# Performance work log

Measured on AMD Instinct MI355X. Metric: run time of the kernel, lower is better.

The kernel has to match this reference:

```python
import jax, jax.numpy as jnp
import numpy as np

B, NP, FIN = 128, 64, 2048   # graphs, nodes per graph, input feat
H, D = 8, 64                 # GAT heads, per-head dim
HD = H * D                   # 512
HID = 1024                   # Set2Set channels (concat of two 512 convs)
R2 = 16.0                    # radius^2 (r=4)
SLOPE = 0.2                  # GATConv leaky_relu slope
EPS = 0.1                    # BatchNorm eps


def setup_inputs() -> dict:
    key = jax.random.key(0)
    ks = jax.random.split(key, 20)
    s = 0.02
    inp = {}
    inp['x'] = jax.random.normal(ks[0], (B * NP, FIN), jnp.float32)
    inp['pos'] = jax.random.uniform(ks[1], (B * NP, 2), jnp.float32) * 20.0
    inp['batch'] = jnp.repeat(jnp.arange(B, dtype=jnp.int32), NP)
    # lin01: Linear(2048,2048,bias=False) + BN(2048, eps=0.1) (eval mode)
    inp['W0'] = jax.random.normal(ks[2], (FIN, 2048), jnp.float32) * s
    inp['bn0_g'] = jnp.ones((2048,), jnp.float32)
    inp['bn0_b'] = jnp.zeros((2048,), jnp.float32)
    inp['bn0_m'] = jnp.zeros((2048,), jnp.float32)
    inp['bn0_v'] = jnp.ones((2048,), jnp.float32)
    # two GATConv(2048, 64, heads=8)
    inp['Wg1'] = jax.random.normal(ks[3], (2048, HD), jnp.float32) * s
    inp['as1'] = jax.random.normal(ks[4], (H, D), jnp.float32) * s
    inp['ad1'] = jax.random.normal(ks[5], (H, D), jnp.float32) * s
    inp['b1'] = jnp.zeros((HD,), jnp.float32)
    inp['Wg2'] = jax.random.normal(ks[6], (2048, HD), jnp.float32) * s
    inp['as2'] = jax.random.normal(ks[7], (H, D), jnp.float32) * s
    inp['ad2'] = jax.random.normal(ks[8], (H, D), jnp.float32) * s
    inp['b2'] = jnp.zeros((HD,), jnp.float32)
    # Set2Set LSTM: 2 layers, input 2*HID, hidden HID
    inp['Wih0'] = jax.random.normal(ks[9], (4 * HID, 2 * HID), jnp.float32) * s
    inp['Whh0'] = jax.random.normal(ks[10], (4 * HID, HID), jnp.float32) * s
    inp['bih0'] = jnp.zeros((4 * HID,), jnp.float32)
    inp['bhh0'] = jnp.zeros((4 * HID,), jnp.float32)
    inp['Wih1'] = jax.random.normal(ks[11], (4 * HID, HID), jnp.float32) * s
    inp['Whh1'] = jax.random.normal(ks[12], (4 * HID, HID), jnp.float32) * s
    inp['bih1'] = jnp.zeros((4 * HID,), jnp.float32)
    inp['bhh1'] = jnp.zeros((4 * HID,), jnp.float32)
    # lin2: Linear(2048,1024,bias=False) + BN(1024, eps=0.1)
    inp['W2'] = jax.random.normal(ks[13], (2 * HID, HID), jnp.float32) * s
    inp['bn2_g'] = jnp.ones((HID,), jnp.float32)
    inp['bn2_b'] = jnp.zeros((HID,), jnp.float32)
    inp['bn2_m'] = jnp.zeros((HID,), jnp.float32)
    inp['bn2_v'] = jnp.ones((HID,), jnp.float32)
    # lin3: Linear(1024, 10)
    inp['W3'] = jax.random.normal(ks[14], (HID, 10), jnp.float32) * s
    inp['b3'] = jnp.zeros((10,), jnp.float32)
    return inp


def _bn(x, g, b, m, v):
    return (x - m) * jax.lax.rsqrt(v + EPS) * g + b


def _gat(xb, adj, Wg, a_src, a_dst, bias):
    # xb: [B, NP, 2048], adj: [B, NP, NP] bool (diag True = self-loops)
    h = (xb @ Wg).reshape(B, NP, H, D)
    es = jnp.einsum('bnhd,hd->bnh', h, a_src)   # source-node score
    ed = jnp.einsum('bnhd,hd->bnh', h, a_dst)   # target-node score
    # e[b, i, j, h]: edge j -> i
    e = jax.nn.leaky_relu(ed[:, :, None, :] + es[:, None, :, :], SLOPE)
    e = jnp.where(adj[..., None], e, -jnp.inf)
    alpha = jax.nn.softmax(e, axis=2)           # softmax over neighbors j
    out = jnp.einsum('bijh,bjhd->bihd', alpha, h).reshape(B, NP, HD)
    return out + bias


def _cell(inp, h, c, Wih, Whh, bih, bhh):
    z = inp @ Wih.T + h @ Whh.T + bih + bhh
    i, f, g, o = jnp.split(z, 4, axis=-1)
    c = jax.nn.sigmoid(f) * c + jax.nn.sigmoid(i) * jnp.tanh(g)
    return jax.nn.sigmoid(o) * jnp.tanh(c), c


def _forward(x, pos, W0, bn0_g, bn0_b, bn0_m, bn0_v,
             Wg1, as1, ad1, b1, Wg2, as2, ad2, b2,
             Wih0, Whh0, bih0, bhh0, Wih1, Whh1, bih1, bhh1,
             W2, bn2_g, bn2_b, bn2_m, bn2_v, W3, b3):
    # radius_graph(r=4) per graph; GATConv re-adds self-loops -> diag True
    p = pos.reshape(B, NP, 2)
    d2 = jnp.sum((p[:, :, None, :] - p[:, None, :, :]) ** 2, axis=-1)
    adj = d2 <= R2
    x = _bn(jax.nn.relu(x @ W0), bn0_g, bn0_b, bn0_m, bn0_v)  # dropout: eval
    xb = x.reshape(B, NP, 2048)
    g1 = jax.nn.relu(_gat(xb, adj, Wg1, as1, ad1, b1))
    g2 = jax.nn.relu(_gat(xb, adj, Wg2, as2, ad2, b2))
    x2 = jnp.concatenate([g1, g2], axis=-1)                   # [B, NP, 1024]
    # Set2Set: processing_steps=2, 2-layer LSTM
    q_star = jnp.zeros((B, 2 * HID), x2.dtype)
    h0 = c0 = h1 = c1 = jnp.zeros((B, HID), x2.dtype)
    for _ in range(2):
        h0, c0 = _cell(q_star, h0, c0, Wih0, Whh0, bih0, bhh0)
        h1, c1 = _cell(h0, h1, c1, Wih1, Whh1, bih1, bhh1)
        e = jnp.einsum('bnd,bd->bn', x2, h1)
        a = jax.nn.softmax(e, axis=1)                         # per-graph softmax
        r = jnp.einsum('bn,bnd->bd', a, x2)
        q_star = jnp.concatenate([h1, r], axis=-1)            # [B, 2048]
    y = _bn(jax.nn.relu(q_star @ W2), bn2_g, bn2_b, bn2_m, bn2_v)
    return y @ W3 + b3                                        # [B, 10] ('A2')


def reference(x, pos, batch, W0, bn0_g, bn0_b, bn0_m, bn0_v,
              Wg1, as1, ad1, b1, Wg2, as2, ad2, b2,
              Wih0, Whh0, bih0, bhh0, Wih1, Whh1, bih1, bhh1,
              W2, bn2_g, bn2_b, bn2_m, bn2_v, W3, b3):
    # batch ids are implicit in the fixed [B, NP] layout
    return _forward(x, pos, W0, bn0_g, bn0_b, bn0_m, bn0_v,
                    Wg1, as1, ad1, b1, Wg2, as2, ad2, b2,
                    Wih0, Whh0, bih0, bhh0, Wih1, Whh1, bih1, bhh1,
                    W2, bn2_g, bn2_b, bn2_m, bn2_v, W3, b3)
```

## Files before the change

kernel.cpp:

```cpp
#include <hip/hip_runtime.h>
#include <hip/hip_bf16.h>

typedef unsigned short u16;
typedef __attribute__((ext_vector_type(8))) short short8;
typedef __attribute__((ext_vector_type(4))) float f32x4;
typedef unsigned long long u64;

#define DI __device__ __forceinline__

DI u16 f2b(float f){
  unsigned u = __float_as_uint(f);
  unsigned r = 0x7fffu + ((u >> 16) & 1u);
  return (u16)((u + r) >> 16);
}
DI float b2f(u16 u){ return __uint_as_float((unsigned)u << 16); }

DI void gl_lds16(const void* g, void* l){
  __builtin_amdgcn_global_load_lds((const __attribute__((address_space(1))) void*)g,
                                   (__attribute__((address_space(3))) void*)l, 16, 0, 0);
}

constexpr size_t O_XBF = 0;
constexpr size_t O_W0T = O_XBF + 33554432;
constexpr size_t O_WGT = O_W0T + 8388608;
constexpr size_t O_W2T = O_WGT + 4194304;
constexpr size_t O_XB  = O_W2T + 4194304;
constexpr size_t O_H   = O_XB  + 33554432;
constexpr size_t O_ES  = O_H   + 33554432;
constexpr size_t O_ED  = O_ES  + 524288;
constexpr size_t O_ADJ = O_ED  + 524288;
constexpr size_t O_SC0 = O_ADJ + 65536;
constexpr size_t O_SH0 = O_SC0 + 8192;
constexpr size_t O_SC2 = O_SH0 + 8192;
constexpr size_t O_SH2 = O_SC2 + 4096;
constexpr size_t O_LB0 = O_SH2 + 4096;
constexpr size_t O_LB1 = O_LB0 + 16384;
constexpr size_t S_AC0 = 0;
constexpr size_t S_AC1 = S_AC0 + 786432;
constexpr size_t S_C0  = S_AC1 + 524288;
constexpr size_t S_C1  = S_C0  + 524288;
constexpr size_t S_H1F = S_C1  + 524288;
constexpr size_t S_ZP  = S_H1F + 524288;
constexpr size_t S_E   = S_ZP  + 16777216;
constexpr size_t S_Z1U = S_E   + 32768;

__global__ __launch_bounds__(256) void setup_all(
    const float* __restrict__ x,
    const float* __restrict__ W0, const float* __restrict__ Wg1,
    const float* __restrict__ Wg2, const float* __restrict__ W2,
    const float* __restrict__ g0, const float* __restrict__ b0, const float* __restrict__ m0, const float* __restrict__ v0,
    const float* __restrict__ g2, const float* __restrict__ b2, const float* __restrict__ m2, const float* __restrict__ v2,
    const float* __restrict__ bih0, const float* __restrict__ bhh0,
    const float* __restrict__ bih1, const float* __restrict__ bhh1,
    const float* __restrict__ pos,
    u16* __restrict__ xbf, u16* __restrict__ w0t, u16* __restrict__ wgt, u16* __restrict__ w2t,
    float* __restrict__ sc0, float* __restrict__ sh0, float* __restrict__ sc2, float* __restrict__ sh2,
    float* __restrict__ lb0, float* __restrict__ lb1, u64* __restrict__ adjm)
{
  __shared__ float tile[32][33];
  __shared__ float px[4][64], py[4][64];
  int bx = blockIdx.x, t = threadIdx.x;
  if(bx < 8192){
    int idx = bx * 256 + t;
    int r = idx >> 8, c8 = (idx & 255) << 3;
    const float* src = x + (size_t)r * 2048 + c8;
    float4 v0 = *(const float4*)src;
    float4 v1 = *(const float4*)(src + 4);
    short8 ov;
    ov[0] = (short)f2b(v0.x); ov[1] = (short)f2b(v0.y); ov[2] = (short)f2b(v0.z); ov[3] = (short)f2b(v0.w);
    ov[4] = (short)f2b(v1.x); ov[5] = (short)f2b(v1.y); ov[6] = (short)f2b(v1.z); ov[7] = (short)f2b(v1.w);
    *(short8*)(xbf + (size_t)r * 2048 + c8) = ov;
  } else if(bx < 16384){
    int bx2 = bx - 8192;
    int cx = bx2 & 127, by = bx2 >> 7;
    const float* src; u16* dst; int C, droff;
    if(cx < 64){      src = W0;  dst = w0t; C = 2048; droff = 0; }
    else if(cx < 80){ src = Wg1; dst = wgt; C = 512;  droff = 0;   cx -= 64; }
    else if(cx < 96){ src = Wg2; dst = wgt; C = 512;  droff = 512; cx -= 80; }
    else {            src = W2;  dst = w2t; C = 1024; droff = 0;   cx -= 96; }
    int c0 = cx * 32, r0 = by * 32;
    int tx = t & 31, ty = t >> 5;
    for(int i = 0; i < 4; i++)
      tile[ty + 8*i][tx] = src[(size_t)(r0 + ty + 8*i) * C + c0 + tx];
    __syncthreads();
    for(int i = 0; i < 4; i++)
      dst[(size_t)(droff + c0 + ty + 8*i) * 2048 + r0 + tx] = f2b(tile[tx][ty + 8*i]);
  } else if(bx < 16400){
    int tt = (bx - 16384) * 256 + t;
    if(tt < 2048){ float s = g0[tt] * rsqrtf(v0[tt] + 0.1f); sc0[tt] = s; sh0[tt] = b0[tt] - m0[tt] * s; }
    if(tt < 1024){ float s = g2[tt] * rsqrtf(v2[tt] + 0.1f); sc2[tt] = s; sh2[tt] = b2[tt] - m2[tt] * s; }
    lb0[tt] = bih0[tt] + bhh0[tt];
    lb1[tt] = bih1[tt] + bhh1[tt];
  } else {
    int w = t >> 6, l = t & 63;
    int g = (bx - 16400) * 4 + w;
    float2 p = ((const float2*)pos)[g * 64 + l];
    px[w][l] = p.x; py[w][l] = p.y;
    __syncthreads();
    float xi = p.x, yi = p.y;
    u64 m = 0;
    for(int j = 0; j < 64; j++){
      float dx = xi - px[w][j], dy = yi - py[w][j];
      if(dx * dx + dy * dy <= 16.0f) m |= (1ull << j);
    }
    adjm[g * 64 + l] = m;
  }
}

#define STAGE_A(buf, half, kt)                                                        \
  { _Pragma("unroll")                                                                 \
    for(int ld = 0; ld < 2; ld++){                                                    \
      int u = ld * 512 + t;                                                           \
      int r = (u >> 3) + (half) * 128, c = u & 7;                                     \
      gl_lds16(A + (size_t)(m0 + r) * K + (kt) * 64 + ((c ^ (r & 7)) << 3),           \
               LA + (buf) * 16384 + ((half) * 1024 + u) * 8);                         \
    } }
#define STAGE_B(buf, half, kt)                                                        \
  { _Pragma("unroll")                                                                 \
    for(int ld = 0; ld < 2; ld++){                                                    \
      int u = ld * 512 + t;                                                           \
      int r = (u >> 3) + (half) * 128, c = u & 7;                                     \
      gl_lds16(Bt + (size_t)(n0 + r) * K + (kt) * 64 + ((c ^ (r & 7)) << 3),          \
               LB + (buf) * 16384 + ((half) * 1024 + u) * 8);                         \
    } }
#define COMPUTE(buf, q)                                                               \
  { if((q) == 0){                                                                     \
      _Pragma("unroll")                                                               \
      for(int nb = 0; nb < 4; nb++)                                                   \
        _Pragma("unroll")                                                             \
        for(int k2 = 0; k2 < 2; k2++){                                                \
          int col = wn + nb * 16 + (l & 15);                                          \
          int kc = k2 * 4 + (l >> 4);                                                 \
          bfr[nb][k2] = Bp[(buf) * 2048 + col * 8 + (kc ^ (col & 7))];                \
        }                                                                             \
    }                                                                                 \
    short8 af[2][2];                                                                  \
    _Pragma("unroll")                                                                 \
    for(int rb = 0; rb < 2; rb++)                                                     \
      _Pragma("unroll")                                                               \
      for(int k2 = 0; k2 < 2; k2++){                                                  \
        int row = wm + (q) * 32 + rb * 16 + (l & 15);                                 \
        int kc = k2 * 4 + (l >> 4);                                                   \
        af[rb][k2] = Ap[(buf) * 2048 + row * 8 + (kc ^ (row & 7))];                   \
      }                                                                               \
    _Pragma("unroll")                                                                 \
    for(int rb = 0; rb < 2; rb++)                                                     \
      _Pragma("unroll")                                                               \
      for(int nb = 0; nb < 4; nb++)                                                   \
        _Pragma("unroll")                                                             \
        for(int k2 = 0; k2 < 2; k2++)                                                 \
          acc[(q) * 2 + rb][nb] = __builtin_amdgcn_mfma_f32_16x16x32_bf16(            \
              af[rb][k2], bfr[nb][k2], acc[(q) * 2 + rb][nb], 0, 0, 0);               \
  }
#define PHASE_BAR() { __builtin_amdgcn_s_barrier(); __builtin_amdgcn_sched_barrier(0); }
#define VM4() { asm volatile("s_waitcnt vmcnt(4)" ::: "memory"); __builtin_amdgcn_sched_barrier(0); }

__global__ __launch_bounds__(512, 2) void gemm8p(
    const u16* __restrict__ A, const u16* __restrict__ Bt, u16* __restrict__ Cb,
    const float* __restrict__ p1, const float* __restrict__ p2,
    int M, int N, int K)
{
  __shared__ alignas(16) u16 LA[2 * 16384];
  __shared__ alignas(16) u16 LB[2 * 16384];
  int m0 = blockIdx.x * 256, n0 = blockIdx.y * 256;
  int t = threadIdx.x, w = t >> 6, l = t & 63;
  int wm = (w >> 2) * 128, wn = (w & 3) * 64;
  int nt = K >> 6, ni = nt >> 1;
  f32x4 acc[8][4];
  #pragma unroll
  for(int a = 0; a < 8; a++)
    #pragma unroll
    for(int b = 0; b < 4; b++) acc[a][b] = {0.f, 0.f, 0.f, 0.f};
  short8 bfr[4][2];
  const short8* Ap = (const short8*)LA;
  const short8* Bp = (const short8*)LB;

  STAGE_A(0, 0, 0); STAGE_A(0, 1, 0); STAGE_B(0, 0, 0); STAGE_B(0, 1, 0);
  STAGE_B(1, 0, 1); STAGE_B(1, 1, 1);
  VM4();
  PHASE_BAR();

  for(int i = 0; i < ni; i++){
    int t1 = 2 * i + 1;
    int t2 = (2 * i + 2 < nt) ? 2 * i + 2 : nt - 1;
    int t3 = (2 * i + 3 < nt) ? 2 * i + 3 : nt - 1;
    STAGE_A(1, 0, t1); STAGE_A(1, 1, t1);
    COMPUTE(0, 0);
    PHASE_BAR();
    STAGE_B(0, 0, t2);
    COMPUTE(0, 1);
    PHASE_BAR();
    STAGE_B(0, 1, t2);
    COMPUTE(0, 2);
    PHASE_BAR();
    COMPUTE(0, 3);
    VM4();
    PHASE_BAR();
    STAGE_A(0, 0, t2);
    COMPUTE(1, 0);
    PHASE_BAR();
    STAGE_A(0, 1, t2);
    COMPUTE(1, 1);
    PHASE_BAR();
    STAGE_B(1, 0, t3);
    COMPUTE(1, 2);
    PHASE_BAR();
    STAGE_B(1, 1, t3);
    COMPUTE(1, 3);
    VM4();
    PHASE_BAR();
  }
  asm volatile("s_waitcnt vmcnt(0)" ::: "memory");

  int cc = n0 + wn + (l & 15);
  int r4 = (l >> 4) << 2;
  #pragma unroll
  for(int ar = 0; ar < 8; ar++)
    #pragma unroll
    for(int nb = 0; nb < 4; nb++)
      #pragma unroll
      for(int r = 0; r < 4; r++){
        int row = m0 + wm + ar * 16 + r4 + r, col = cc + nb * 16;
        float v = acc[ar][nb][r];
        v = fmaxf(v, 0.f) * p1[col] + p2[col];
        Cb[(size_t)row * N + col] = f2b(v);
      }
}

template<int MODE>
__global__ __launch_bounds__(256) void gemm_bf16(
    const u16* __restrict__ A, const u16* __restrict__ Bt,
    float* __restrict__ Cf, u16* __restrict__ Cb,
    const float* __restrict__ p1, const float* __restrict__ p2,
    int M, int N, int K)
{
  constexpr int BM = 128, BN = 128, BK = 64;
  __shared__ alignas(16) u16 Al[BM * BK];
  __shared__ alignas(16) u16 Bl[BN * BK];
  int m0 = blockIdx.x * BM, n0 = blockIdx.y * BN;
  int t = threadIdx.x, w = t >> 6, l = t & 63;
  int wm = (w >> 1) * 64, wn = (w & 1) * 64;
  f32x4 acc[4][4];
  for(int a = 0; a < 4; a++) for(int b = 0; b < 4; b++) acc[a][b] = {0.f, 0.f, 0.f, 0.f};

  const short8* Ap = (const short8*)Al;
  const short8* Bp = (const short8*)Bl;

  for(int k0 = 0; k0 < K; k0 += BK){
    #pragma unroll
    for(int u = t; u < BM * 8; u += 256){
      int r = u >> 3, c = u & 7;
      gl_lds16(A + (size_t)(m0 + r) * K + k0 + ((c ^ (r & 7)) << 3), Al + u * 8);
    }
    #pragma unroll
    for(int u = t; u < BN * 8; u += 256){
      int r = u >> 3, c = u & 7;
      gl_lds16(Bt + (size_t)(n0 + r) * K + k0 + ((c ^ (r & 7)) << 3), Bl + u * 8);
    }
    __syncthreads();
    #pragma unroll
    for(int ks = 0; ks < 2; ks++){
      int kc = ks * 4 + (l >> 4);
      short8 av[4], bv[4];
      #pragma unroll
      for(int mi = 0; mi < 4; mi++){ int r = wm + mi * 16 + (l & 15); av[mi] = Ap[r * 8 + (kc ^ (r & 7))]; }
      #pragma unroll
      for(int ni = 0; ni < 4; ni++){ int r = wn + ni * 16 + (l & 15); bv[ni] = Bp[r * 8 + (kc ^ (r & 7))]; }
      #pragma unroll
      for(int mi = 0; mi < 4; mi++)
        #pragma unroll
        for(int ni = 0; ni < 4; ni++)
          acc[mi][ni] = __builtin_amdgcn_mfma_f32_16x16x32_bf16(av[mi], bv[ni], acc[mi][ni], 0, 0, 0);
    }
    __syncthreads();
  }

  int cr = m0 + wm + ((l >> 4) << 2);
  int cc = n0 + wn + (l & 15);
  for(int mi = 0; mi < 4; mi++)
    for(int ni = 0; ni < 4; ni++)
      for(int r = 0; r < 4; r++){
        int row = cr + mi * 16 + r, col = cc + ni * 16;
        float v = acc[mi][ni][r];
        if(MODE == 1){ v = fmaxf(v, 0.f) * p1[col] + p2[col]; Cb[(size_t)row * N + col] = f2b(v); }
        else if(MODE == 3){ Cb[(size_t)row * N + col] = f2b(v); }
        else { Cf[(size_t)row * N + col] = v; }
      }
}

__global__ __launch_bounds__(256) void gemm_sk(
    const u16* __restrict__ A, const u16* __restrict__ Bt, float* __restrict__ Cf,
    int N, int lda, int ldb, int kPer)
{
  constexpr int BM = 128, BN = 64, BK = 64;
  __shared__ alignas(16) u16 Al[BM * BK];
  __shared__ alignas(16) u16 Bl[BN * BK];
  int n0 = blockIdx.x * BN;
  int kb = blockIdx.y * kPer;
  float* C = Cf + (size_t)blockIdx.y * 128 * N;
  int t = threadIdx.x, w = t >> 6, l = t & 63;
  int wm = (w >> 1) * 64, wn = (w & 1) * 32;
  f32x4 acc[4][2];
  for(int a = 0; a < 4; a++) for(int b = 0; b < 2; b++) acc[a][b] = {0.f, 0.f, 0.f, 0.f};

  const short8* Ap = (const short8*)Al;
  const short8* Bp = (const short8*)Bl;

  for(int k0 = kb; k0 < kb + kPer; k0 += BK){
    #pragma unroll
    for(int u = t; u < BM * 8; u += 256){
      int r = u >> 3, c = u & 7;
      gl_lds16(A + (size_t)r * lda + k0 + ((c ^ (r & 7)) << 3), Al + u * 8);
    }
    #pragma unroll
    for(int u = t; u < BN * 8; u += 256){
      int r = u >> 3, c = u & 7;
      gl_lds16(Bt + (size_t)(n0 + r) * ldb + k0 + ((c ^ (r & 7)) << 3), Bl + u * 8);
    }
    __syncthreads();
    #pragma unroll
    for(int ks = 0; ks < 2; ks++){
      int kc = ks * 4 + (l >> 4);
      short8 av[4], bv[2];
      #pragma unroll
      for(int mi = 0; mi < 4; mi++){ int r = wm + mi * 16 + (l & 15); av[mi] = Ap[r * 8 + (kc ^ (r & 7))]; }
      #pragma unroll
      for(int ni = 0; ni < 2; ni++){ int r = wn + ni * 16 + (l & 15); bv[ni] = Bp[r * 8 + (kc ^ (r & 7))]; }
      #pragma unroll
      for(int mi = 0; mi < 4; mi++)
        #pragma unroll
        for(int ni = 0; ni < 2; ni++)
          acc[mi][ni] = __builtin_amdgcn_mfma_f32_16x16x32_bf16(av[mi], bv[ni], acc[mi][ni], 0, 0, 0);
    }
    __syncthreads();
  }

  int cr = wm + ((l >> 4) << 2);
  int cc = n0 + wn + (l & 15);
  for(int mi = 0; mi < 4; mi++)
    for(int ni = 0; ni < 2; ni++)
      for(int r = 0; r < 4; r++)
        C[(size_t)(cr + mi * 16 + r) * N + cc + ni * 16] = acc[mi][ni][r];
}

__global__ __launch_bounds__(256) void gemm_skf(
    const u16* __restrict__ A, const float* __restrict__ Wih, const float* __restrict__ Whh,
    float* __restrict__ Cf, int N, int lda, int Kih, int Khh, int kPer)
{
  constexpr int BM = 128, BN = 64, BK = 64;
  __shared__ alignas(16) u16 Al[BM * BK];
  __shared__ alignas(16) u16 Bl[BN * BK];
  int n0 = blockIdx.x * BN;
  int kb = blockIdx.y * kPer;
  float* C = Cf + (size_t)blockIdx.y * 128 * N;
  int t = threadIdx.x, w = t >> 6, l = t & 63;
  int wm = (w >> 1) * 64, wn = (w & 1) * 32;
  f32x4 acc[4][2];
  for(int a = 0; a < 4; a++) for(int b = 0; b < 2; b++) acc[a][b] = {0.f, 0.f, 0.f, 0.f};

  const short8* Ap = (const short8*)Al;
  const short8* Bp = (const short8*)Bl;

  for(int k0 = kb; k0 < kb + kPer; k0 += BK){
    #pragma unroll
    for(int u = t; u < BM * 8; u += 256){
      int r = u >> 3, c = u & 7;
      gl_lds16(A + (size_t)r * lda + k0 + ((c ^ (r & 7)) << 3), Al + u * 8);
    }
    #pragma unroll
    for(int u = t; u < BN * 8; u += 256){
      int r = u >> 3, c = u & 7;
      int gk = k0 + c * 8;
      const float* src = (gk < Kih) ? (Wih + (size_t)(n0 + r) * Kih + gk)
                                    : (Whh + (size_t)(n0 + r) * Khh + (gk - Kih));
      float4 v0 = *(const float4*)src;
      float4 v1 = *(const float4*)(src + 4);
      short8 ov;
      ov[0] = (short)f2b(v0.x); ov[1] = (short)f2b(v0.y); ov[2] = (short)f2b(v0.z); ov[3] = (short)f2b(v0.w);
      ov[4] = (short)f2b(v1.x); ov[5] = (short)f2b(v1.y); ov[6] = (short)f2b(v1.z); ov[7] = (short)f2b(v1.w);
      ((short8*)Bl)[r * 8 + (c ^ (r & 7))] = ov;
    }
    __syncthreads();
    #pragma unroll
    for(int ks = 0; ks < 2; ks++){
      int kc = ks * 4 + (l >> 4);
      short8 av[4], bv[2];
      #pragma unroll
      for(int mi = 0; mi < 4; mi++){ int r = wm + mi * 16 + (l & 15); av[mi] = Ap[r * 8 + (kc ^ (r & 7))]; }
      #pragma unroll
      for(int ni = 0; ni < 2; ni++){ int r = wn + ni * 16 + (l & 15); bv[ni] = Bp[r * 8 + (kc ^ (r & 7))]; }
      #pragma unroll
      for(int mi = 0; mi < 4; mi++)
        #pragma unroll
        for(int ni = 0; ni < 2; ni++)
          acc[mi][ni] = __builtin_amdgcn_mfma_f32_16x16x32_bf16(av[mi], bv[ni], acc[mi][ni], 0, 0, 0);
    }
    __syncthreads();
  }

  int cr = wm + ((l >> 4) << 2);
  int cc = n0 + wn + (l & 15);
  for(int mi = 0; mi < 4; mi++)
    for(int ni = 0; ni < 2; ni++)
      for(int r = 0; r < 4; r++)
        C[(size_t)(cr + mi * 16 + r) * N + cc + ni * 16] = acc[mi][ni][r];
}

__global__ __launch_bounds__(256) void gat_attn2(const u64* __restrict__ adjm,
    const u16* __restrict__ h,
    const float* __restrict__ as1, const float* __restrict__ ad1,
    const float* __restrict__ as2, const float* __restrict__ ad2,
    const float* __restrict__ b1, const float* __restrict__ b2,
    u16* __restrict__ x2b){
  int b = blockIdx.x;
  int cv = blockIdx.y >> 3, hh = blockIdx.y & 7;
  __shared__ float hst[64][64];
  __shared__ float esl[64], edl[64];
  __shared__ u64 adjs[64];
  int t = threadIdx.x, w = t >> 6, l = t & 63;
  {
    int j = t >> 2, d0 = (t & 3) * 16;
    const u16* hr = h + (size_t)(b * 64 + j) * 1024 + cv * 512 + hh * 64 + d0;
    #pragma unroll
    for(int k = 0; k < 16; k++) hst[j][d0 + k] = b2f(hr[k]);
  }
  if(t < 64) adjs[t] = adjm[b * 64 + t];
  __syncthreads();
  float aSl = ((cv ? as2 : as1) + hh * 64)[l];
  float aDl = ((cv ? ad2 : ad1) + hh * 64)[l];
  for(int it = 0; it < 16; it++){
    int j = it * 4 + w;
    float v = hst[j][l];
    float ps = v * aSl, pd = v * aDl;
    for(int o = 32; o; o >>= 1){ ps += __shfl_xor(ps, o); pd += __shfl_xor(pd, o); }
    if(l == 0){ esl[j] = ps; edl[j] = pd; }
  }
  __syncthreads();
  float alphaR[16];
  #pragma unroll
  for(int it = 0; it < 16; it++){
    int i = it * 4 + w;
    bool on = (adjs[i] >> l) & 1;
    float e = edl[i] + esl[l];
    e = e > 0.f ? e : 0.2f * e;
    float mx = on ? e : -1e30f;
    for(int o = 32; o; o >>= 1) mx = fmaxf(mx, __shfl_xor(mx, o));
    float p = on ? __expf(e - mx) : 0.f;
    float s = p;
    for(int o = 32; o; o >>= 1) s += __shfl_xor(s, o);
    alphaR[it] = p / s;
  }
  float accv[16];
  #pragma unroll
  for(int k = 0; k < 16; k++) accv[k] = 0.f;
  #pragma unroll
  for(int j = 0; j < 64; j++){
    float hv = hst[j][l];
    #pragma unroll
    for(int it = 0; it < 16; it++){
      float av = __uint_as_float(__builtin_amdgcn_readlane(__float_as_uint(alphaR[it]), j));
      accv[it] += av * hv;
    }
  }
  float bl = ((cv ? b2 : b1) + hh * 64)[l];
  #pragma unroll
  for(int it = 0; it < 16; it++){
    int i = it * 4 + w;
    x2b[(size_t)(b * 64 + i) * 1024 + cv * 512 + hh * 64 + l] = f2b(fmaxf(accv[it] + bl, 0.f));
  }
}

__global__ __launch_bounds__(256) void s2s0_gemv(const float* __restrict__ Wih1,
    const float* __restrict__ lb1, const float* __restrict__ lb0, float* __restrict__ z1u){
  __shared__ float hs[1024];
  int t = threadIdx.x;
  for(int i = t; i < 1024; i += 256){
    float zi = lb0[i], zg = lb0[2048 + i], zo = lb0[3072 + i];
    float cn = (1.f / (1.f + __expf(-zi))) * tanhf(zg);
    hs[i] = (1.f / (1.f + __expf(-zo))) * tanhf(cn);
  }
  __syncthreads();
  int w = t >> 6, l = t & 63;
  int r = blockIdx.x * 4 + w;
  const float* wr = Wih1 + (size_t)r * 1024;
  float s = 0.f;
  #pragma unroll
  for(int k = 0; k < 16; k++) s += wr[l + 64 * k] * hs[l + 64 * k];
  for(int o = 32; o; o >>= 1) s += __shfl_xor(s, o);
  if(l == 0) z1u[r] = s + lb1[r];
}

__global__ void lstm_gate0(const float* __restrict__ zp, const float* __restrict__ lb,
                           float* __restrict__ c, u16* __restrict__ ac0, u16* __restrict__ ac1,
                           int ns){
  int t = blockIdx.x * 256 + threadIdx.x;
  int b = t >> 10, j = t & 1023;
  size_t base = (size_t)b * 4096;
  float zi = 0, zf = 0, zg = 0, zo = 0;
  for(int s = 0; s < ns; s++){
    const float* zr = zp + (size_t)s * 524288 + base;
    zi += zr[j]; zf += zr[1024 + j]; zg += zr[2048 + j]; zo += zr[3072 + j];
  }
  zi += lb[j]; zf += lb[1024 + j]; zg += lb[2048 + j]; zo += lb[3072 + j];
  float ci = c[t];
  float si = 1.f / (1.f + __expf(-zi)), sf = 1.f / (1.f + __expf(-zf)), so = 1.f / (1.f + __expf(-zo));
  float cn = sf * ci + si * tanhf(zg);
  c[t] = cn;
  u16 hb = f2b(so * tanhf(cn));
  ac0[(size_t)b * 3072 + 2048 + j] = hb;
  ac1[(size_t)b * 2048 + j] = hb;
}

__global__ void lstm_gate1(const float* __restrict__ zp, const float* __restrict__ lb,
                           float* __restrict__ c, float* __restrict__ h1f,
                           u16* __restrict__ ac1, u16* __restrict__ ac0, int ns){
  int t = blockIdx.x * 256 + threadIdx.x;
  int b = t >> 10, j = t & 1023;
  size_t base = (size_t)b * 4096;
  float zi = 0, zf = 0, zg = 0, zo = 0;
  for(int s = 0; s < ns; s++){
    const float* zr = zp + (size_t)s * 524288 + base;
    zi += zr[j]; zf += zr[1024 + j]; zg += zr[2048 + j]; zo += zr[3072 + j];
  }
  zi += lb[j]; zf += lb[1024 + j]; zg += lb[2048 + j]; zo += lb[3072 + j];
  float ci = c[t];
  float si = 1.f / (1.f + __expf(-zi)), sf = 1.f / (1.f + __expf(-zf)), so = 1.f / (1.f + __expf(-zo));
  float cn = sf * ci + si * tanhf(zg);
  c[t] = cn;
  float hn = so * tanhf(cn);
  h1f[t] = hn;
  u16 hb = f2b(hn);
  ac1[(size_t)b * 2048 + 1024 + j] = hb;
  ac0[(size_t)b * 3072 + j] = hb;
}

template<int STEP>
__global__ __launch_bounds__(256) void s2s_e(const u16* __restrict__ x2b,
    const float* __restrict__ h1, const float* __restrict__ z1u, float* __restrict__ e){
  __shared__ float h1s[1024];
  int t = threadIdx.x, w = t >> 6, l = t & 63;
  int node = blockIdx.x * 4 + w;
  int b = node >> 6;
  for(int i = t; i < 1024; i += 256){
    if(STEP == 0){
      float zi = z1u[i], zg = z1u[2048 + i], zo = z1u[3072 + i];
      float cn = (1.f / (1.f + __expf(-zi))) * tanhf(zg);
      h1s[i] = (1.f / (1.f + __expf(-zo))) * tanhf(cn);
    } else {
      h1s[i] = h1[(size_t)b * 1024 + i];
    }
  }
  __syncthreads();
  const u16* xr = x2b + (size_t)node * 1024;
  float s = 0.f;
  #pragma unroll
  for(int k = 0; k < 16; k++){
    int d = k * 64 + l;
    s += b2f(xr[d]) * h1s[d];
  }
  for(int o = 32; o; o >>= 1) s += __shfl_xor(s, o);
  if(l == 0) e[node] = s;
}

template<int STEP>
__global__ __launch_bounds__(256) void s2s_r(const u16* __restrict__ x2b,
    const float* __restrict__ e, u16* __restrict__ ac0,
    const float* __restrict__ lb0, const float* __restrict__ z1u,
    u16* __restrict__ ac1, float* __restrict__ c0b, float* __restrict__ c1b){
  int b = blockIdx.x, sl = blockIdx.y;
  __shared__ float al[64];
  int t = threadIdx.x;
  if(t < 64){
    float v = e[b * 64 + t];
    float mx = v;
    for(int o = 32; o; o >>= 1) mx = fmaxf(mx, __shfl_xor(mx, o));
    float p = __expf(v - mx);
    float ss = p;
    for(int o = 32; o; o >>= 1) ss += __shfl_xor(ss, o);
    al[t] = p / ss;
  }
  __syncthreads();
  int d = sl * 256 + t;
  const u16* xp = x2b + (size_t)b * 65536 + d;
  float r = 0.f;
  #pragma unroll 8
  for(int j = 0; j < 64; j++) r += al[j] * b2f(xp[j * 1024]);
  ac0[(size_t)b * 3072 + 1024 + d] = f2b(r);
  if(STEP == 0){
    float zi0 = lb0[d], zg0 = lb0[2048 + d], zo0 = lb0[3072 + d];
    float c0 = (1.f / (1.f + __expf(-zi0))) * tanhf(zg0);
    float h0 = (1.f / (1.f + __expf(-zo0))) * tanhf(c0);
    float zi1 = z1u[d], zg1 = z1u[2048 + d], zo1 = z1u[3072 + d];
    float c1 = (1.f / (1.f + __expf(-zi1))) * tanhf(zg1);
    float h1 = (1.f / (1.f + __expf(-zo1))) * tanhf(c1);
    c0b[(size_t)b * 1024 + d] = c0;
    c1b[(size_t)b * 1024 + d] = c1;
    u16 h0b = f2b(h0), h1b = f2b(h1);
    ac0[(size_t)b * 3072 + d] = h1b;
    ac0[(size_t)b * 3072 + 2048 + d] = h0b;
    ac1[(size_t)b * 2048 + d] = h0b;
    ac1[(size_t)b * 2048 + 1024 + d] = h1b;
  }
}

__global__ __launch_bounds__(256) void lin3(const float* __restrict__ zp2,
    const float* __restrict__ sc2, const float* __restrict__ sh2,
    const float* __restrict__ W3, const float* __restrict__ b3, float* __restrict__ out){
  int b = blockIdx.x;
  __shared__ float yl[1024];
  int t = threadIdx.x, w = t >> 6, l = t & 63;
  for(int d = t; d < 1024; d += 256){
    float v = 0.f;
    for(int s = 0; s < 8; s++) v += zp2[(size_t)s * 131072 + b * 1024 + d];
    yl[d] = fmaxf(v, 0.f) * sc2[d] + sh2[d];
  }
  __syncthreads();
  for(int n = w; n < 10; n += 4){
    float s = 0.f;
    for(int d = l; d < 1024; d += 64) s += yl[d] * W3[d * 10 + n];
    for(int o = 32; o; o >>= 1) s += __shfl_xor(s, o);
    if(l == 0) out[b * 10 + n] = s + b3[n];
  }
}

extern "C" void kernel_launch(void* const* d_in, const int* in_sizes, int n_in,
                              void* d_out, int out_size, void* d_ws, size_t ws_size,
                              hipStream_t stream){
  const float* x    = (const float*)d_in[0];
  const float* pos  = (const float*)d_in[1];
  const float* W0   = (const float*)d_in[3];
  const float* bn0g = (const float*)d_in[4];
  const float* bn0b = (const float*)d_in[5];
  const float* bn0m = (const float*)d_in[6];
  const float* bn0v = (const float*)d_in[7];
  const float* Wg1  = (const float*)d_in[8];
  const float* as1  = (const float*)d_in[9];
  const float* ad1  = (const float*)d_in[10];
  const float* b1   = (const float*)d_in[11];
  const float* Wg2  = (const float*)d_in[12];
  const float* as2  = (const float*)d_in[13];
  const float* ad2  = (const float*)d_in[14];
  const float* b2   = (const float*)d_in[15];
  const float* Wih0 = (const float*)d_in[16];
  const float* Whh0 = (const float*)d_in[17];
  const float* bih0 = (const float*)d_in[18];
  const float* bhh0 = (const float*)d_in[19];
  const float* Wih1 = (const float*)d_in[20];
  const float* Whh1 = (const float*)d_in[21];
  const float* bih1 = (const float*)d_in[22];
  const float* bhh1 = (const float*)d_in[23];
  const float* W2   = (const float*)d_in[24];
  const float* bn2g = (const float*)d_in[25];
  const float* bn2b = (const float*)d_in[26];
  const float* bn2m = (const float*)d_in[27];
  const float* bn2v = (const float*)d_in[28];
  const float* W3   = (const float*)d_in[29];
  const float* b3   = (const float*)d_in[30];

  char* ws = (char*)d_ws;
  u16*   xbf  = (u16*)(ws + O_XBF);
  u16*   x2b  = (u16*)(ws + O_XBF);
  u16*   w0t  = (u16*)(ws + O_W0T);
  u16*   wgt  = (u16*)(ws + O_WGT);
  u16*   w2t  = (u16*)(ws + O_W2T);
  u16*   xb   = (u16*)(ws + O_XB);
  u16*   hb   = (u16*)(ws + O_H);
  u64*   adjm = (u64*)(ws + O_ADJ);
  float* sc0  = (float*)(ws + O_SC0);
  float* sh0  = (float*)(ws + O_SH0);
  float* sc2  = (float*)(ws + O_SC2);
  float* sh2  = (float*)(ws + O_SH2);
  float* lb0  = (float*)(ws + O_LB0);
  float* lb1  = (float*)(ws + O_LB1);
  char*  s2sb = ws + O_H;
  u16*   ac0  = (u16*)(s2sb + S_AC0);
  u16*   ac1  = (u16*)(s2sb + S_AC1);
  float* c0b  = (float*)(s2sb + S_C0);
  float* c1b  = (float*)(s2sb + S_C1);
  float* h1f  = (float*)(s2sb + S_H1F);
  float* zp   = (float*)(s2sb + S_ZP);
  float* ebuf = (float*)(s2sb + S_E);
  float* z1u  = (float*)(s2sb + S_Z1U);

  setup_all<<<16432, 256, 0, stream>>>(x, W0, Wg1, Wg2, W2,
                                       bn0g, bn0b, bn0m, bn0v, bn2g, bn2b, bn2m, bn2v,
                                       bih0, bhh0, bih1, bhh1, pos,
                                       xbf, w0t, wgt, w2t, sc0, sh0, sc2, sh2, lb0, lb1, adjm);

  gemm8p<<<dim3(32, 8), 512, 0, stream>>>(xbf, w0t, xb, sc0, sh0, 8192, 2048, 2048);
  gemm_bf16<3><<<dim3(64, 8), 256, 0, stream>>>(xb, wgt, nullptr, hb, nullptr, nullptr, 8192, 1024, 2048);
  gat_attn2<<<dim3(128, 16), 256, 0, stream>>>(adjm, hb, as1, ad1, as2, ad2, b1, b2, x2b);

  s2s0_gemv<<<1024, 256, 0, stream>>>(Wih1, lb1, lb0, z1u);
  s2s_e<0><<<2048, 256, 0, stream>>>(x2b, nullptr, z1u, ebuf);
  s2s_r<0><<<dim3(128, 4), 256, 0, stream>>>(x2b, ebuf, ac0, lb0, z1u, ac1, c0b, c1b);

  gemm_skf<<<dim3(64, 8), 256, 0, stream>>>(ac0, Wih0, Whh0, zp, 4096, 3072, 2048, 1024, 384);
  lstm_gate0<<<512, 256, 0, stream>>>(zp, lb0, c0b, ac0, ac1, 8);
  gemm_skf<<<dim3(64, 8), 256, 0, stream>>>(ac1, Wih1, Whh1, zp, 4096, 2048, 1024, 1024, 256);
  lstm_gate1<<<512, 256, 0, stream>>>(zp, lb1, c1b, h1f, ac1, ac0, 8);
  s2s_e<1><<<2048, 256, 0, stream>>>(x2b, h1f, nullptr, ebuf);
  s2s_r<1><<<dim3(128, 4), 256, 0, stream>>>(x2b, ebuf, ac0, nullptr, nullptr, nullptr, nullptr, nullptr);

  gemm_sk<<<dim3(16, 8), 256, 0, stream>>>(ac0, w2t, zp, 1024, 3072, 2048, 256);
  lin3<<<128, 256, 0, stream>>>(zp, sc2, sh2, W3, b3, (float*)d_out);
}
```

Before: 278.2 us.

## Replace GAT projection GEMM with double-buffered 256x128 pipelined kernel

Replaces the simple single-buffered 128x128 bf16 GEMM used for the GAT feature projection with a 512-thread, 256x128-tile kernel that double-buffers A and B in LDS and interleaves async global-to-LDS loads with MFMA phases under fine-grained barriers and vmcnt waits. The goal is to hide global load latency behind compute and raise arithmetic intensity per block, in the style of the existing gemm8p kernel. In exchange it uses more LDS and registers per block, and the grid shrinks to 256 blocks, which could underfill the GPU.

```diff
diff --git a/kernel.cpp b/kernel.cpp
--- a/kernel.cpp
+++ b/kernel.cpp
@@ -227,64 +227,116 @@
       }
 }
 
-template<int MODE>
-__global__ __launch_bounds__(256) void gemm_bf16(
-    const u16* __restrict__ A, const u16* __restrict__ Bt,
-    float* __restrict__ Cf, u16* __restrict__ Cb,
-    const float* __restrict__ p1, const float* __restrict__ p2,
+#define STAGE_A2(buf, half, kt)                                                       \
+  { _Pragma("unroll")                                                                 \
+    for(int ld = 0; ld < 2; ld++){                                                    \
+      int u = ld * 512 + t;                                                           \
+      int r = (u >> 3) + (half) * 128, c = u & 7;                                     \
+      gl_lds16(A + (size_t)(m0 + r) * K + (kt) * 64 + ((c ^ (r & 7)) << 3),           \
+               LA + (buf) * 16384 + ((half) * 1024 + u) * 8);                         \
+    } }
+#define STAGE_B2(buf, half, kt)                                                       \
+  { int u = t;                                                                        \
+    int r = (u >> 3) + (half) * 64, c = u & 7;                                        \
+    gl_lds16(Bt + (size_t)(n0 + r) * K + (kt) * 64 + ((c ^ (r & 7)) << 3),            \
+             LB + (buf) * 8192 + ((half) * 512 + u) * 8); }
+#define COMPUTE2(buf, q)                                                              \
+  { if((q) == 0){                                                                     \
+      _Pragma("unroll")                                                               \
+      for(int nb = 0; nb < 2; nb++)                                                   \
+        _Pragma("unroll")                                                             \
+        for(int k2 = 0; k2 < 2; k2++){                                                \
+          int col = wn + nb * 16 + (l & 15);                                          \
+          int kc = k2 * 4 + (l >> 4);                                                 \
+          bfr[nb][k2] = Bp[(buf) * 1024 + col * 8 + (kc ^ (col & 7))];                \
+        }                                                                             \
+    }                                                                                 \
+    short8 af[2][2];                                                                  \
+    _Pragma("unroll")                                                                 \
+    for(int rb = 0; rb < 2; rb++)                                                     \
+      _Pragma("unroll")                                                               \
+      for(int k2 = 0; k2 < 2; k2++){                                                  \
+        int row = wm + (q) * 32 + rb * 16 + (l & 15);                                 \
+        int kc = k2 * 4 + (l >> 4);                                                   \
+        af[rb][k2] = Ap[(buf) * 2048 + row * 8 + (kc ^ (row & 7))];                   \
+      }                                                                               \
+    _Pragma("unroll")                                                                 \
+    for(int rb = 0; rb < 2; rb++)                                                     \
+      _Pragma("unroll")                                                               \
+      for(int nb = 0; nb < 2; nb++)                                                   \
+        _Pragma("unroll")                                                             \
+        for(int k2 = 0; k2 < 2; k2++)                                                 \
+          acc[(q) * 2 + rb][nb] = __builtin_amdgcn_mfma_f32_16x16x32_bf16(            \
+              af[rb][k2], bfr[nb][k2], acc[(q) * 2 + rb][nb], 0, 0, 0);               \
+  }
+#define VM2() { asm volatile("s_waitcnt vmcnt(2)" ::: "memory"); __builtin_amdgcn_sched_barrier(0); }
+
+__global__ __launch_bounds__(512, 2) void gemm8pB(
+    const u16* __restrict__ A, const u16* __restrict__ Bt, u16* __restrict__ Cb,
     int M, int N, int K)
 {
-  constexpr int BM = 128, BN = 128, BK = 64;
-  __shared__ alignas(16) u16 Al[BM * BK];
-  __shared__ alignas(16) u16 Bl[BN * BK];
-  int m0 = blockIdx.x * BM, n0 = blockIdx.y * BN;
+  __shared__ alignas(16) u16 LA[2 * 16384];
+  __shared__ alignas(16) u16 LB[2 * 8192];
+  int m0 = blockIdx.x * 256, n0 = blockIdx.y * 128;
   int t = threadIdx.x, w = t >> 6, l = t & 63;
-  int wm = (w >> 1) * 64, wn = (w & 1) * 64;
-  f32x4 acc[4][4];
-  for(int a = 0; a < 4; a++) for(int b = 0; b < 4; b++) acc[a][b] = {0.f, 0.f, 0.f, 0.f};
-
-  const short8* Ap = (const short8*)Al;
-  const short8* Bp = (const short8*)Bl;
-
-  for(int k0 = 0; k0 < K; k0 += BK){
-    #pragma unroll
-    for(int u = t; u < BM * 8; u += 256){
-      int r = u >> 3, c = u & 7;
-      gl_lds16(A + (size_t)(m0 + r) * K + k0 + ((c ^ (r & 7)) << 3), Al + u * 8);
-    }
-    #pragma unroll
-    for(int u = t; u < BN * 8; u += 256){
-      int r = u >> 3, c = u & 7;
-      gl_lds16(Bt + (size_t)(n0 + r) * K + k0 + ((c ^ (r & 7)) << 3), Bl + u * 8);
-    }
-    __syncthreads();
-    #pragma unroll
-    for(int ks = 0; ks < 2; ks++){
-      int kc = ks * 4 + (l >> 4);
-      short8 av[4], bv[4];
+  int wm = (w >> 2) * 128, wn = (w & 3) * 32;
+  int nt = K >> 6, ni = nt >> 1;
+  f32x4 acc[8][2];
+  #pragma unroll
+  for(int a = 0; a < 8; a++)
+    #pragma unroll
+    for(int b = 0; b < 2; b++) acc[a][b] = {0.f, 0.f, 0.f, 0.f};
+  short8 bfr[2][2];
+  const short8* Ap = (const short8*)LA;
+  const short8* Bp = (const short8*)LB;
+
+  STAGE_A2(0, 0, 0); STAGE_A2(0, 1, 0); STAGE_B2(0, 0, 0); STAGE_B2(0, 1, 0);
+  STAGE_B2(1, 0, 1); STAGE_B2(1, 1, 1);
+  VM2();
+  PHASE_BAR();
+
+  for(int i = 0; i < ni; i++){
+    int t1 = 2 * i + 1;
+    int t2 = (2 * i + 2 < nt) ? 2 * i + 2 : nt - 1;
+    int t3 = (2 * i + 3 < nt) ? 2 * i + 3 : nt - 1;
+    STAGE_A2(1, 0, t1); STAGE_A2(1, 1, t1);
+    COMPUTE2(0, 0);
+    PHASE_BAR();
+    STAGE_B2(0, 0, t2);
+    COMPUTE2(0, 1);
+    PHASE_BAR();
+    STAGE_B2(0, 1, t2);
+    COMPUTE2(0, 2);
+    PHASE_BAR();
+    COMPUTE2(0, 3);
+    VM2();
+    PHASE_BAR();
+    STAGE_A2(0, 0, t2);
+    COMPUTE2(1, 0);
+    PHASE_BAR();
+    STAGE_A2(0, 1, t2);
+    COMPUTE2(1, 1);
+    PHASE_BAR();
+    STAGE_B2(1, 0, t3);
+    COMPUTE2(1, 2);
+    PHASE_BAR();
+    STAGE_B2(1, 1, t3);
+    COMPUTE2(1, 3);
+    VM2();
+    PHASE_BAR();
+  }
+  asm volatile("s_waitcnt vmcnt(0)" ::: "memory");
+
+  int cc = n0 + wn + (l & 15);
+  int r4 = (l >> 4) << 2;
+  #pragma unroll
+  for(int ar = 0; ar < 8; ar++)
+    #pragma unroll
+    for(int nb = 0; nb < 2; nb++)
       #pragma unroll
-      for(int mi = 0; mi < 4; mi++){ int r = wm + mi * 16 + (l & 15); av[mi] = Ap[r * 8 + (kc ^ (r & 7))]; }
-      #pragma unroll
-      for(int ni = 0; ni < 4; ni++){ int r = wn + ni * 16 + (l & 15); bv[ni] = Bp[r * 8 + (kc ^ (r & 7))]; }
-      #pragma unroll
-      for(int mi = 0; mi < 4; mi++)
-        #pragma unroll
-        for(int ni = 0; ni < 4; ni++)
-          acc[mi][ni] = __builtin_amdgcn_mfma_f32_16x16x32_bf16(av[mi], bv[ni], acc[mi][ni], 0, 0, 0);
-    }
-    __syncthreads();
-  }
-
-  int cr = m0 + wm + ((l >> 4) << 2);
-  int cc = n0 + wn + (l & 15);
-  for(int mi = 0; mi < 4; mi++)
-    for(int ni = 0; ni < 4; ni++)
       for(int r = 0; r < 4; r++){
-        int row = cr + mi * 16 + r, col = cc + ni * 16;
-        float v = acc[mi][ni][r];
-        if(MODE == 1){ v = fmaxf(v, 0.f) * p1[col] + p2[col]; Cb[(size_t)row * N + col] = f2b(v); }
-        else if(MODE == 3){ Cb[(size_t)row * N + col] = f2b(v); }
-        else { Cf[(size_t)row * N + col] = v; }
+        int row = m0 + wm + ar * 16 + r4 + r, col = cc + nb * 16;
+        Cb[(size_t)row * N + col] = f2b(acc[ar][nb][r]);
       }
 }
 
@@ -688,7 +740,7 @@
                                        xbf, w0t, wgt, w2t, sc0, sh0, sc2, sh2, lb0, lb1, adjm);
 
   gemm8p<<<dim3(32, 8), 512, 0, stream>>>(xbf, w0t, xb, sc0, sh0, 8192, 2048, 2048);
-  gemm_bf16<3><<<dim3(64, 8), 256, 0, stream>>>(xb, wgt, nullptr, hb, nullptr, nullptr, 8192, 1024, 2048);
+  gemm8pB<<<dim3(32, 8), 512, 0, stream>>>(xb, wgt, hb, 8192, 1024, 2048);
   gat_attn2<<<dim3(128, 16), 256, 0, stream>>>(adjm, hb, as1, ad1, as2, ad2, b1, b2, x2b);
 
   s2s0_gemv<<<1024, 256, 0, stream>>>(Wih1, lb1, lb0, z1u);
```

New measurement: 280.0 us. Within noise of the previous version (+0.7%).
